# Optimization experiments

Measured on AMD Instinct MI355X. Metric: run time of the kernel, lower is better.

## Reference

```python
import jax, jax.numpy as jnp
import numpy as np
from jax import lax

THRESHOLD = 0.7
OUT = 224  # output size of nn.Upsample(size=(224,224), mode='bilinear', align_corners=True)


def _bilinear(img, xs, ys):
    """align_corners=True bilinear sampling. img: (..., H, W); xs: (oh,), ys: (ow,) float coords."""
    H, W = img.shape[-2], img.shape[-1]
    x0 = jnp.clip(jnp.floor(xs).astype(jnp.int32), 0, H - 1)
    x1 = jnp.clip(x0 + 1, 0, H - 1)
    y0 = jnp.clip(jnp.floor(ys).astype(jnp.int32), 0, W - 1)
    y1 = jnp.clip(y0 + 1, 0, W - 1)
    wx = (xs - x0.astype(xs.dtype))[:, None]  # (oh,1)
    wy = (ys - y0.astype(ys.dtype))[None, :]  # (1,ow)
    top = jnp.take(img, x0, axis=-2)
    bot = jnp.take(img, x1, axis=-2)
    v00 = jnp.take(top, y0, axis=-1)
    v01 = jnp.take(top, y1, axis=-1)
    v10 = jnp.take(bot, y0, axis=-1)
    v11 = jnp.take(bot, y1, axis=-1)
    return (1 - wx) * ((1 - wy) * v00 + wy * v01) + wx * ((1 - wy) * v10 + wy * v11)


def _normalize01(h):
    n = h.shape[0]
    f = h.reshape(n, -1)
    mn = f.min(axis=1, keepdims=True)
    mx = f.max(axis=1, keepdims=True)
    return ((f - mn) / (mx - mn)).reshape(h.shape)


def _largest_cc(mask):
    """8-connected (skimage connectivity=2) largest component via min-label propagation.
    mask: (N,H,W) bool -> (N,H,W) bool, True on the largest connected component."""
    N, H, W = mask.shape
    BIG = H * W  # background sentinel label
    idx = jnp.arange(BIG, dtype=jnp.int32).reshape(1, H, W)
    lab0 = jnp.where(mask, idx, BIG)

    def body(state):
        lab, _ = state
        pooled = lax.reduce_window(lab, jnp.int32(BIG), lax.min, (1, 3, 3), (1, 1, 1), 'SAME')
        new = jnp.where(mask, pooled, BIG)
        return new, jnp.any(new != lab)

    lab, _ = lax.while_loop(lambda s: s[1], body, (lab0, jnp.bool_(True)))

    def counts(l):
        return jnp.zeros(BIG + 1, jnp.int32).at[l.reshape(-1)].add(1)

    c = jax.vmap(counts)(lab)                 # (N, H*W+1); last bin = background
    best = jnp.argmax(c[:, :BIG], axis=1)     # label of largest foreground component
    return lab == best[:, None, None]


def _bbox(lcc):
    N, H, W = lcc.shape
    rows = lcc.any(axis=2)
    cols = lcc.any(axis=1)
    has = rows.any(axis=1)
    xmin = jnp.argmax(rows, axis=1).astype(jnp.int32)
    xmax = (H - 1 - jnp.argmax(rows[:, ::-1], axis=1)).astype(jnp.int32)
    ymin = jnp.argmax(cols, axis=1).astype(jnp.int32)
    ymax = (W - 1 - jnp.argmax(cols[:, ::-1], axis=1)).astype(jnp.int32)
    # fallback to full image if the mask is empty (torch code would crash here)
    xmin = jnp.where(has, xmin, 0)
    ymin = jnp.where(has, ymin, 0)
    xmax = jnp.where(has, xmax, H - 1)
    ymax = jnp.where(has, ymax, W - 1)
    return xmin, xmax, ymin, ymax


def _crop_resize(images, xmin, xmax, ymin, ymax):
    # torch crop is images[i][:, xmin:xmax, ymin:ymax] (exclusive upper), then align_corners resize
    grid = jnp.arange(OUT, dtype=jnp.float32) / (OUT - 1)

    def one(img, a, b, c, d):
        Lx = jnp.maximum(b - a, 1)
        Ly = jnp.maximum(d - c, 1)
        xs = a.astype(jnp.float32) + grid * (Lx - 1).astype(jnp.float32)
        ys = c.astype(jnp.float32) + grid * (Ly - 1).astype(jnp.float32)
        return _bilinear(img, xs, ys)

    return jax.vmap(one)(images, xmin, xmax, ymin, ymax)


def setup_inputs() -> dict:
    key = jax.random.key(0)
    k1, k2 = jax.random.split(key)
    x = jax.random.normal(k1, (64, 3, 224, 224), dtype=jnp.float32)
    features = jax.random.normal(k2, (64, 2048, 7, 7), dtype=jnp.float32)
    return {"x": x, "features": features}


def reference(x, features):
    # distance = normalize01(Lmax(features, axis=1))
    heat = _normalize01(jnp.max(jnp.abs(features), axis=1))       # (N, h, w)
    h, w = heat.shape[1], heat.shape[2]
    grid = jnp.arange(OUT, dtype=jnp.float32) / (OUT - 1)
    out_heatmap = _bilinear(heat, grid * (h - 1), grid * (w - 1))  # (N, 224, 224)
    mask = out_heatmap > THRESHOLD
    lcc = _largest_cc(mask)
    xmin, xmax, ymin, ymax = _bbox(lcc)
    crop = _crop_resize(x, xmin, xmax, ymin, ymax)                 # (N, 3, 224, 224)
    coords = jnp.stack([ymin, xmin, ymax, xmax], axis=1)           # (N, 4), torch coord order
    return crop, out_heatmap, coords
```

## Files before the change

kernel.cpp:

```cpp
#include <hip/hip_runtime.h>
#include <stdint.h>

#define NIMG   64
#define NCH    2048
#define HW7    49
#define OUTW   224
#define NPIX   50176
#define CROP_N 9633792
#define HEAT_OFF  9633792
#define COORD_OFF 12845056
#define THRESH 0.7f

#define MAXR 8
#define RCAP (224*MAXR)
#define NWORDS 784
#define WPAD   788

#define NGRP 16

#define MASKW_BYTE_OFF 262144
#define CNT_BYTE_OFF   665600

__global__ __launch_bounds__(256) void k1_heat(const float* __restrict__ F,
                                               float* __restrict__ heatPart,
                                               unsigned* __restrict__ imgCnt) {
    __shared__ float smax[4][64];
    const int t = threadIdx.x;
    const int b = blockIdx.x;
    if (b == 0 && t < NIMG) {
        __hip_atomic_store(&imgCnt[t], 0u, __ATOMIC_RELAXED, __HIP_MEMORY_SCOPE_AGENT);
    }
    const int n = b >> 4, g = b & 15;
    const int w = t >> 6, l = t & 63;
    const int lp = (l < HW7) ? l : 0;
    const float* base = F + (size_t)n * 100352 + (size_t)(g * 128 + w) * HW7 + lp;
    float vmax = 0.0f;
#pragma unroll 8
    for (int i = 0; i < 32; ++i) {
        vmax = fmaxf(vmax, fabsf(base[(size_t)i * 4 * HW7]));
    }
    smax[w][l] = vmax;
    __syncthreads();
    if (t < HW7) {
        float m = fmaxf(fmaxf(smax[0][t], smax[1][t]), fmaxf(smax[2][t], smax[3][t]));
        heatPart[b * HW7 + t] = m;
    }
}

__device__ inline unsigned uf_find(volatile unsigned* P, unsigned x) {
    while (true) {
        unsigned p = P[x];
        if (p == x) return x;
        unsigned gp = P[p];
        if (gp == p) return p;
        P[x] = gp;
        x = gp;
    }
}

__device__ inline void uf_merge(volatile unsigned* P, unsigned a, unsigned b) {
    while (true) {
        a = uf_find(P, a); b = uf_find(P, b);
        if (a == b) return;
        if (a > b) { unsigned tmp = a; a = b; b = tmp; }
        unsigned old = atomicCAS((unsigned*)&P[b], b, a);
        if (old == b) return;
        b = old;
    }
}

__global__ __launch_bounds__(256) void k2_heatmask(const float* __restrict__ heatPart,
                                                   float* __restrict__ heatOut,
                                                   unsigned long long* __restrict__ maskW,
                                                   unsigned* __restrict__ imgCnt,
                                                   float* __restrict__ coords) {
#pragma clang fp contract(off)
    __shared__ float raw[HW7];
    __shared__ float h7[HW7];
    __shared__ float s_mn, s_mx;
    __shared__ float wT[OUTW];
    __shared__ int   i0T[OUTW];
    __shared__ int   i1T[OUTW];
    __shared__ int   s_last;
    __shared__ unsigned long long W[WPAD];
    __shared__ unsigned short runS[RCAP], runE[RCAP];
    __shared__ unsigned char nRuns[224];
    __shared__ unsigned parent[RCAP], cnt[RCAP];
    __shared__ unsigned rmin[RCAP], rmax[RCAP], cmin[RCAP], cmax[RCAP];
    __shared__ unsigned bestScore, bestRid;

    const int t = threadIdx.x;
    const int b = blockIdx.x;
    const int n = b >> 3, slice = b & 7;

    if (t < HW7) {
        float m = heatPart[(n * NGRP + 0) * HW7 + t];
#pragma unroll
        for (int g = 1; g < NGRP; ++g) m = fmaxf(m, heatPart[(n * NGRP + g) * HW7 + t]);
        raw[t] = m;
    }
    if (t < OUTW) {
        float gx = (float)t / 223.0f;
        float xs = gx * 6.0f;
        int x0 = (int)floorf(xs); x0 = min(max(x0, 0), 6);
        i0T[t] = x0;
        i1T[t] = min(x0 + 1, 6);
        wT[t]  = xs - (float)x0;
    }
    __syncthreads();
    if (t == 0) {
        float mn = raw[0], mx = raw[0];
        for (int i = 1; i < HW7; ++i) { float v = raw[i]; mn = fminf(mn, v); mx = fmaxf(mx, v); }
        s_mn = mn; s_mx = mx;
    }
    __syncthreads();
    if (t < HW7) h7[t] = (raw[t] - s_mn) / (s_mx - s_mn);
    __syncthreads();

    const int pbase = slice * 6272;
    for (int k = 0; k < 25; ++k) {
        int pl = k * 256 + t;
        if (pl < 6272) {
            int p = pbase + pl;
            int i = p / 224, j = p - i * 224;
            int x0 = i0T[i], x1 = i1T[i];
            int y0 = i0T[j], y1 = i1T[j];
            float wx = wT[i], wy = wT[j];
            float v00 = h7[x0 * 7 + y0], v01 = h7[x0 * 7 + y1];
            float v10 = h7[x1 * 7 + y0], v11 = h7[x1 * 7 + y1];
            float val = (1.0f - wx) * ((1.0f - wy) * v00 + wy * v01)
                      + wx * ((1.0f - wy) * v10 + wy * v11);
            heatOut[(size_t)n * NPIX + p] = val;
            unsigned long long bal = __ballot(val > THRESH);
            if ((t & 63) == 0) {
                __hip_atomic_store(&maskW[(size_t)n * WPAD + (p >> 6)], bal,
                                   __ATOMIC_RELAXED, __HIP_MEMORY_SCOPE_AGENT);
            }
        }
    }

    __syncthreads();
    if (t == 0) {
        unsigned old = __hip_atomic_fetch_add(&imgCnt[n], 1u,
                                              __ATOMIC_ACQ_REL, __HIP_MEMORY_SCOPE_AGENT);
        s_last = (old == 7u);
    }
    __syncthreads();
    if (!s_last) return;

    for (int i = t; i < NWORDS; i += 256)
        W[i] = __hip_atomic_load(&maskW[(size_t)n * WPAD + i],
                                 __ATOMIC_RELAXED, __HIP_MEMORY_SCOPE_AGENT);
    if (t < WPAD - NWORDS) W[NWORDS + t] = 0ull;
    for (int i = t; i < RCAP; i += 256) {
        parent[i] = (unsigned)i; cnt[i] = 0u;
        rmin[i] = 0xFFFFFFFFu; rmax[i] = 0u; cmin[i] = 0xFFFFFFFFu; cmax[i] = 0u;
    }
    if (t == 0) { bestScore = 0u; bestRid = 0u; }
    __syncthreads();

    if (t < 224) {
        const int r = t;
        const int bit0 = r * 224;
        const int w0 = bit0 >> 6, sh = bit0 & 63;
        unsigned long long rb[4];
#pragma unroll
        for (int q = 0; q < 4; ++q) {
            unsigned long long lo = W[w0 + q] >> sh;
            unsigned long long hi = sh ? (W[w0 + q + 1] << (64 - sh)) : 0ull;
            rb[q] = lo | hi;
        }
        rb[3] &= 0xFFFFFFFFull;

        unsigned long long st[4], en[4];
        unsigned long long carry = 0ull;
#pragma unroll
        for (int q = 0; q < 4; ++q) {
            unsigned long long shl = (rb[q] << 1) | carry;
            carry = rb[q] >> 63;
            st[q] = rb[q] & ~shl;
        }
#pragma unroll
        for (int q = 0; q < 4; ++q) {
            unsigned long long nxt = (q < 3) ? rb[q + 1] : 0ull;
            en[q] = rb[q] & ~((rb[q] >> 1) | (nxt << 63));
        }
        int ns = 0;
#pragma unroll
        for (int q = 0; q < 4; ++q) {
            unsigned long long x = st[q];
            while (x) {
                int z = __builtin_ctzll(x); x &= x - 1;
                if (ns < MAXR) runS[r * MAXR + ns] = (unsigned short)(q * 64 + z);
                ns++;
            }
        }
        int ne = 0;
#pragma unroll
        for (int q = 0; q < 4; ++q) {
            unsigned long long x = en[q];
            while (x) {
                int z = __builtin_ctzll(x); x &= x - 1;
                if (ne < MAXR) runE[r * MAXR + ne] = (unsigned short)(q * 64 + z);
                ne++;
            }
        }
        nRuns[r] = (unsigned char)min(ns, MAXR);
    }
    __syncthreads();

    if (t >= 1 && t < 224) {
        const int r = t;
        const int na = nRuns[r], nb = nRuns[r - 1];
        for (int k = 0; k < na; ++k) {
            int rid = r * MAXR + k;
            int s = runS[rid], e = runE[rid];
            for (int m = 0; m < nb; ++m) {
                int qid = (r - 1) * MAXR + m;
                int s2 = runS[qid], e2 = runE[qid];
                if (s2 <= e + 1 && e2 >= s - 1) uf_merge(parent, (unsigned)rid, (unsigned)qid);
            }
        }
    }
    __syncthreads();

    for (int rid = t; rid < RCAP; rid += 256) {
        int r = rid >> 3, k = rid & (MAXR - 1);
        if (k < (int)nRuns[r]) {
            int s = runS[rid], e = runE[rid];
            unsigned root = uf_find(parent, (unsigned)rid);
            atomicAdd(&cnt[root], (unsigned)(e - s + 1));
            atomicMin(&rmin[root], (unsigned)r);
            atomicMax(&rmax[root], (unsigned)r);
            atomicMin(&cmin[root], (unsigned)s);
            atomicMax(&cmax[root], (unsigned)e);
        }
    }
    __syncthreads();

    for (int rid = t; rid < RCAP; rid += 256) {
        unsigned c = cnt[rid];
        if (c > 0u) {
            unsigned label = (unsigned)((rid >> 3) * 224 + (int)runS[rid]);
            unsigned score = (c << 16) | (65535u - label);
            atomicMax(&bestScore, score);
        }
    }
    __syncthreads();
    for (int rid = t; rid < RCAP; rid += 256) {
        unsigned c = cnt[rid];
        if (c > 0u) {
            unsigned label = (unsigned)((rid >> 3) * 224 + (int)runS[rid]);
            unsigned score = (c << 16) | (65535u - label);
            if (score == bestScore) bestRid = (unsigned)rid;
        }
    }
    __syncthreads();

    if (t == 0) {
        int xmin, xmax, ymin, ymax;
        if (bestScore == 0u) {
            xmin = 0; ymin = 0; xmax = 223; ymax = 223;
        } else {
            unsigned rb_ = bestRid;
            xmin = (int)rmin[rb_]; xmax = (int)rmax[rb_];
            ymin = (int)cmin[rb_]; ymax = (int)cmax[rb_];
        }
        coords[n * 4 + 0] = (float)ymin;
        coords[n * 4 + 1] = (float)xmin;
        coords[n * 4 + 2] = (float)ymax;
        coords[n * 4 + 3] = (float)xmax;
    }
}

__global__ __launch_bounds__(256) void k4_crop(const float* __restrict__ X,
                                               const float* __restrict__ coords,
                                               float* __restrict__ out) {
#pragma clang fp contract(off)
    const int t = threadIdx.x;
    const int b = blockIdx.x;
    const int n = b / 49;
    const int p4 = ((b % 49) * 256 + t) * 4;
    const int oi = p4 / 224, oj = p4 - oi * 224;

    int ymin = (int)coords[n * 4 + 0];
    int xmin = (int)coords[n * 4 + 1];
    int ymax = (int)coords[n * 4 + 2];
    int xmax = (int)coords[n * 4 + 3];
    int Lx = max(xmax - xmin, 1);
    int Ly = max(ymax - ymin, 1);

    float gx = (float)oi / 223.0f;
    float xs = (float)xmin + gx * (float)(Lx - 1);
    int x0 = (int)floorf(xs); x0 = min(max(x0, 0), 223); int x1 = min(x0 + 1, 223);
    float wx = xs - (float)x0;

    int   y0q[4], y1q[4];
    float wyq[4];
#pragma unroll
    for (int q = 0; q < 4; ++q) {
        float gy = (float)(oj + q) / 223.0f;
        float ys = (float)ymin + gy * (float)(Ly - 1);
        int y0 = (int)floorf(ys); y0 = min(max(y0, 0), 223);
        y0q[q] = y0; y1q[q] = min(y0 + 1, 223);
        wyq[q] = ys - (float)y0;
    }

    const float* img = X + (size_t)n * 150528;
    float* obase = out + (size_t)n * 150528 + p4;
#pragma unroll
    for (int ch = 0; ch < 3; ++ch) {
        const float* rt = img + ch * NPIX + x0 * 224;
        const float* rb = img + ch * NPIX + x1 * 224;
        float r[4];
#pragma unroll
        for (int q = 0; q < 4; ++q) {
            float v00 = rt[y0q[q]], v01 = rt[y1q[q]];
            float v10 = rb[y0q[q]], v11 = rb[y1q[q]];
            r[q] = (1.0f - wx) * ((1.0f - wyq[q]) * v00 + wyq[q] * v01)
                 + wx * ((1.0f - wyq[q]) * v10 + wyq[q] * v11);
        }
        *reinterpret_cast<float4*>(obase + (size_t)ch * NPIX) =
            make_float4(r[0], r[1], r[2], r[3]);
    }
}

extern "C" void kernel_launch(void* const* d_in, const int* in_sizes, int n_in,
                              void* d_out, int out_size, void* d_ws, size_t ws_size,
                              hipStream_t stream) {
    (void)in_sizes; (void)n_in; (void)out_size; (void)d_ws; (void)ws_size;
    const float* X = (const float*)d_in[0];
    const float* F = (const float*)d_in[1];
    float* out = (float*)d_out;

    float* heatPart = (float*)d_out;
    unsigned long long* maskW = (unsigned long long*)((char*)d_out + MASKW_BYTE_OFF);
    unsigned* imgCnt = (unsigned*)((char*)d_out + CNT_BYTE_OFF);
    float* heatOut = out + HEAT_OFF;
    float* coords  = out + COORD_OFF;

    k1_heat    <<<dim3(1024), dim3(256), 0, stream>>>(F, heatPart, imgCnt);
    k2_heatmask<<<dim3(512),  dim3(256), 0, stream>>>(heatPart, heatOut, maskW, imgCnt, coords);
    k4_crop    <<<dim3(3136), dim3(256), 0, stream>>>(X, coords, out);
}
```

Measured before the change: 153.1 us.

## Split connected-component labeling into its own 1024-thread kernel, one thread per run

Removes the last-block-done atomic counter scheme from the heatmap kernel and moves connected-component labeling into a separate kernel with one 1024-thread block per image. Each run slot now gets its own thread instead of one thread looping over a row's runs, and the per-row run capacity drops from 8 to 4, which shrinks shared memory. This trades an extra kernel launch for shorter serial loops and a lighter heatmap kernel. Rows with more than 4 runs would be truncated, so labeling can go wrong on masks with many fragments per row.

```diff
diff --git a/kernel.cpp b/kernel.cpp
--- a/kernel.cpp
+++ b/kernel.cpp
@@ -11,7 +11,7 @@
 #define COORD_OFF 12845056
 #define THRESH 0.7f
 
-#define MAXR 8
+#define MAXR 4
 #define RCAP (224*MAXR)
 #define NWORDS 784
 #define WPAD   788
@@ -19,17 +19,12 @@
 #define NGRP 16
 
 #define MASKW_BYTE_OFF 262144
-#define CNT_BYTE_OFF   665600
 
 __global__ __launch_bounds__(256) void k1_heat(const float* __restrict__ F,
-                                               float* __restrict__ heatPart,
-                                               unsigned* __restrict__ imgCnt) {
+                                               float* __restrict__ heatPart) {
     __shared__ float smax[4][64];
     const int t = threadIdx.x;
     const int b = blockIdx.x;
-    if (b == 0 && t < NIMG) {
-        __hip_atomic_store(&imgCnt[t], 0u, __ATOMIC_RELAXED, __HIP_MEMORY_SCOPE_AGENT);
-    }
     const int n = b >> 4, g = b & 15;
     const int w = t >> 6, l = t & 63;
     const int lp = (l < HW7) ? l : 0;
@@ -47,33 +42,9 @@
     }
 }
 
-__device__ inline unsigned uf_find(volatile unsigned* P, unsigned x) {
-    while (true) {
-        unsigned p = P[x];
-        if (p == x) return x;
-        unsigned gp = P[p];
-        if (gp == p) return p;
-        P[x] = gp;
-        x = gp;
-    }
-}
-
-__device__ inline void uf_merge(volatile unsigned* P, unsigned a, unsigned b) {
-    while (true) {
-        a = uf_find(P, a); b = uf_find(P, b);
-        if (a == b) return;
-        if (a > b) { unsigned tmp = a; a = b; b = tmp; }
-        unsigned old = atomicCAS((unsigned*)&P[b], b, a);
-        if (old == b) return;
-        b = old;
-    }
-}
-
-__global__ __launch_bounds__(256) void k2_heatmask(const float* __restrict__ heatPart,
-                                                   float* __restrict__ heatOut,
-                                                   unsigned long long* __restrict__ maskW,
-                                                   unsigned* __restrict__ imgCnt,
-                                                   float* __restrict__ coords) {
+__global__ __launch_bounds__(256) void k2_heatmap(const float* __restrict__ heatPart,
+                                                  float* __restrict__ heatOut,
+                                                  unsigned long long* __restrict__ maskW) {
 #pragma clang fp contract(off)
     __shared__ float raw[HW7];
     __shared__ float h7[HW7];
@@ -81,14 +52,6 @@
     __shared__ float wT[OUTW];
     __shared__ int   i0T[OUTW];
     __shared__ int   i1T[OUTW];
-    __shared__ int   s_last;
-    __shared__ unsigned long long W[WPAD];
-    __shared__ unsigned short runS[RCAP], runE[RCAP];
-    __shared__ unsigned char nRuns[224];
-    __shared__ unsigned parent[RCAP], cnt[RCAP];
-    __shared__ unsigned rmin[RCAP], rmax[RCAP], cmin[RCAP], cmax[RCAP];
-    __shared__ unsigned bestScore, bestRid;
-
     const int t = threadIdx.x;
     const int b = blockIdx.x;
     const int n = b >> 3, slice = b & 7;
@@ -132,29 +95,49 @@
                       + wx * ((1.0f - wy) * v10 + wy * v11);
             heatOut[(size_t)n * NPIX + p] = val;
             unsigned long long bal = __ballot(val > THRESH);
-            if ((t & 63) == 0) {
-                __hip_atomic_store(&maskW[(size_t)n * WPAD + (p >> 6)], bal,
-                                   __ATOMIC_RELAXED, __HIP_MEMORY_SCOPE_AGENT);
-            }
-        }
-    }
-
-    __syncthreads();
-    if (t == 0) {
-        unsigned old = __hip_atomic_fetch_add(&imgCnt[n], 1u,
-                                              __ATOMIC_ACQ_REL, __HIP_MEMORY_SCOPE_AGENT);
-        s_last = (old == 7u);
-    }
-    __syncthreads();
-    if (!s_last) return;
-
-    for (int i = t; i < NWORDS; i += 256)
-        W[i] = __hip_atomic_load(&maskW[(size_t)n * WPAD + i],
-                                 __ATOMIC_RELAXED, __HIP_MEMORY_SCOPE_AGENT);
-    if (t < WPAD - NWORDS) W[NWORDS + t] = 0ull;
-    for (int i = t; i < RCAP; i += 256) {
-        parent[i] = (unsigned)i; cnt[i] = 0u;
-        rmin[i] = 0xFFFFFFFFu; rmax[i] = 0u; cmin[i] = 0xFFFFFFFFu; cmax[i] = 0u;
+            if ((t & 63) == 0) maskW[(size_t)n * WPAD + (p >> 6)] = bal;
+        }
+    }
+}
+
+__device__ inline unsigned uf_find(volatile unsigned* P, unsigned x) {
+    while (true) {
+        unsigned p = P[x];
+        if (p == x) return x;
+        unsigned gp = P[p];
+        if (gp == p) return p;
+        P[x] = gp;
+        x = gp;
+    }
+}
+
+__device__ inline void uf_merge(volatile unsigned* P, unsigned a, unsigned b) {
+    while (true) {
+        a = uf_find(P, a); b = uf_find(P, b);
+        if (a == b) return;
+        if (a > b) { unsigned tmp = a; a = b; b = tmp; }
+        unsigned old = atomicCAS((unsigned*)&P[b], b, a);
+        if (old == b) return;
+        b = old;
+    }
+}
+
+__global__ __launch_bounds__(1024) void k3_ccl(const unsigned long long* __restrict__ maskW,
+                                               float* __restrict__ coords) {
+    __shared__ unsigned long long W[WPAD];
+    __shared__ unsigned short runS[RCAP], runE[RCAP];
+    __shared__ unsigned char nRuns[224];
+    __shared__ unsigned parent[RCAP], cnt[RCAP];
+    __shared__ unsigned rmin[RCAP], rmax[RCAP], cmin[RCAP], cmax[RCAP];
+    __shared__ unsigned bestScore, bestRid;
+    const int t = threadIdx.x;
+    const int n = blockIdx.x;
+
+    if (t < NWORDS) W[t] = maskW[(size_t)n * WPAD + t];
+    if (t >= NWORDS && t < WPAD) W[t] = 0ull;
+    if (t < RCAP) {
+        parent[t] = (unsigned)t; cnt[t] = 0u;
+        rmin[t] = 0xFFFFFFFFu; rmax[t] = 0u; cmin[t] = 0xFFFFFFFFu; cmax[t] = 0u;
     }
     if (t == 0) { bestScore = 0u; bestRid = 0u; }
     __syncthreads();
@@ -209,11 +192,11 @@
     }
     __syncthreads();
 
-    if (t >= 1 && t < 224) {
-        const int r = t;
-        const int na = nRuns[r], nb = nRuns[r - 1];
-        for (int k = 0; k < na; ++k) {
-            int rid = r * MAXR + k;
+    if (t >= MAXR && t < RCAP) {
+        const int r = t >> 2, k = t & (MAXR - 1);
+        if (k < (int)nRuns[r]) {
+            const int nb = nRuns[r - 1];
+            int rid = t;
             int s = runS[rid], e = runE[rid];
             for (int m = 0; m < nb; ++m) {
                 int qid = (r - 1) * MAXR + m;
@@ -224,11 +207,11 @@
     }
     __syncthreads();
 
-    for (int rid = t; rid < RCAP; rid += 256) {
-        int r = rid >> 3, k = rid & (MAXR - 1);
+    if (t < RCAP) {
+        int r = t >> 2, k = t & (MAXR - 1);
         if (k < (int)nRuns[r]) {
-            int s = runS[rid], e = runE[rid];
-            unsigned root = uf_find(parent, (unsigned)rid);
+            int s = runS[t], e = runE[t];
+            unsigned root = uf_find(parent, (unsigned)t);
             atomicAdd(&cnt[root], (unsigned)(e - s + 1));
             atomicMin(&rmin[root], (unsigned)r);
             atomicMax(&rmax[root], (unsigned)r);
@@ -238,21 +221,21 @@
     }
     __syncthreads();
 
-    for (int rid = t; rid < RCAP; rid += 256) {
-        unsigned c = cnt[rid];
+    if (t < RCAP) {
+        unsigned c = cnt[t];
         if (c > 0u) {
-            unsigned label = (unsigned)((rid >> 3) * 224 + (int)runS[rid]);
+            unsigned label = (unsigned)((t >> 2) * 224 + (int)runS[t]);
             unsigned score = (c << 16) | (65535u - label);
             atomicMax(&bestScore, score);
         }
     }
     __syncthreads();
-    for (int rid = t; rid < RCAP; rid += 256) {
-        unsigned c = cnt[rid];
+    if (t < RCAP) {
+        unsigned c = cnt[t];
         if (c > 0u) {
-            unsigned label = (unsigned)((rid >> 3) * 224 + (int)runS[rid]);
+            unsigned label = (unsigned)((t >> 2) * 224 + (int)runS[t]);
             unsigned score = (c << 16) | (65535u - label);
-            if (score == bestScore) bestRid = (unsigned)rid;
+            if (score == bestScore) bestRid = (unsigned)t;
         }
     }
     __syncthreads();
@@ -335,11 +318,11 @@
 
     float* heatPart = (float*)d_out;
     unsigned long long* maskW = (unsigned long long*)((char*)d_out + MASKW_BYTE_OFF);
-    unsigned* imgCnt = (unsigned*)((char*)d_out + CNT_BYTE_OFF);
     float* heatOut = out + HEAT_OFF;
     float* coords  = out + COORD_OFF;
 
-    k1_heat    <<<dim3(1024), dim3(256), 0, stream>>>(F, heatPart, imgCnt);
-    k2_heatmask<<<dim3(512),  dim3(256), 0, stream>>>(heatPart, heatOut, maskW, imgCnt, coords);
-    k4_crop    <<<dim3(3136), dim3(256), 0, stream>>>(X, coords, out);
-}
+    k1_heat   <<<dim3(1024), dim3(256),  0, stream>>>(F, heatPart);
+    k2_heatmap<<<dim3(512),  dim3(256),  0, stream>>>(heatPart, heatOut, maskW);
+    k3_ccl    <<<dim3(64),   dim3(1024), 0, stream>>>(maskW, coords);
+    k4_crop   <<<dim3(3136), dim3(256),  0, stream>>>(X, coords, out);
+}
```

New measurement: 138.8 us. 1.1x faster.
